# Kernel tuning notes

Measured on AMD Instinct MI355X. Metric: run time of the kernel, lower is better.

## Reference

```python
import jax, jax.numpy as jnp
import numpy as np

B, N, C = 2, 4096, 192
H = 8
D = C // H  # 24


def setup_inputs() -> dict:
    key = jax.random.key(0)
    k1, k2, k3, k4 = jax.random.split(key, 4)
    x = jax.random.normal(k1, (B, N, C), dtype=jnp.float32)
    # qkv Linear (no bias by default): torch Linear weight is [out, in] -> [3C, C]
    W_qkv = jax.random.normal(k2, (3 * C, C), dtype=jnp.float32) * (1.0 / np.sqrt(C))
    W_proj = jax.random.normal(k3, (C, C), dtype=jnp.float32) * (1.0 / np.sqrt(C))
    b_proj = jax.random.normal(k4, (C,), dtype=jnp.float32) * 0.01
    scale = jnp.asarray(D ** -0.5, dtype=jnp.float32)  # learned scalar, init head_dim**-0.5
    return {"x": x, "W_qkv": W_qkv, "W_proj": W_proj, "b_proj": b_proj, "scale": scale}


def reference(x, W_qkv, W_proj, b_proj, scale):
    b, n, c = x.shape
    h, d = H, c // H
    qkv = jnp.einsum('bnc,oc->bno', x, W_qkv)              # [B,N,3C]
    qkv = qkv.reshape(b, n, 3, h, d).transpose(2, 0, 3, 1, 4)  # [3,B,H,N,D]
    q, k, v = qkv[0], qkv[1], qkv[2]
    # (q_i - k_j).sum(-1) == sum(q_i) - sum(k_j): avoids the [B,H,N,N,D] blowup
    qs = q.sum(-1)                                          # [B,H,N]
    ks = k.sum(-1)                                          # [B,H,N]
    dist = qs[..., :, None] - ks[..., None, :]              # [B,H,N,N]
    attn = jax.nn.softmax(-dist * scale, axis=-1)           # [B,H,N,N]
    out = jnp.einsum('bhij,bhjd->bhid', attn, v)            # [B,H,N,D]
    out = out.transpose(0, 2, 1, 3).reshape(b, n, c)        # [B,N,C]
    return jnp.einsum('bnc,oc->bno', out, W_proj) + b_proj
```

## Files before the change

kernel.cpp:

```cpp
#include <hip/hip_runtime.h>

#define B 2
#define N 4096
#define C 192
#define H 8
#define D 24
#define ROWS 32
#define NCHUNK (B * N / ROWS)
#define PJ 1544

#define PART_OFF 0
#define XW_OFF   395264

__global__ __launch_bounds__(256) void kA(const float* __restrict__ x,
                                          const float* __restrict__ Wqkv,
                                          const float* __restrict__ scale,
                                          float* __restrict__ part) {
    __shared__ __align__(16) float wk[H * 196];
    __shared__ __align__(16) float lx[ROWS * 196];
    __shared__ float le[ROWS * 9];
    const int tid = threadIdx.x;
    const int blk = blockIdx.x;

    for (int i = tid; i < H * C; i += 256) {
        const int h = i / C, c = i - h * C;
        const float* wr = Wqkv + (size_t)(C + h * D) * C + c;
        float s = 0.f;
        #pragma unroll
        for (int d = 0; d < D; ++d) s += wr[d * C];
        wk[h * 196 + c] = s;
    }
    const float4* xb = (const float4*)(x + (size_t)blk * ROWS * C);
    #pragma unroll
    for (int k = 0; k < 6; ++k) {
        const int f4 = tid + k * 256;
        const int r = f4 / 48, c4 = f4 - r * 48;
        *(float4*)&lx[r * 196 + c4 * 4] = xb[f4];
    }
    __syncthreads();

    {
        const int r = tid >> 3, h = tid & 7;
        const float4* xr = (const float4*)&lx[r * 196];
        const float4* wh = (const float4*)&wk[h * 196];
        float acc = 0.f;
        #pragma unroll 8
        for (int c4 = 0; c4 < 48; ++c4) {
            float4 a = xr[c4], w = wh[c4];
            acc += a.x * w.x + a.y * w.y + a.z * w.z + a.w * w.w;
        }
        le[r * 9 + h] = __expf(acc * scale[0]);
    }
    __syncthreads();

    const int h = tid >> 5, c0 = tid & 31;
    float acc[6] = {};
    float zacc = 0.f;
    for (int r = 0; r < ROWS; ++r) {
        const float e = le[r * 9 + h];
        if (c0 == 0) zacc += e;
        #pragma unroll
        for (int j = 0; j < 6; ++j) acc[j] += e * lx[r * 196 + c0 + 32 * j];
    }
    float* pb = part + (size_t)blk * PJ;
    #pragma unroll
    for (int j = 0; j < 6; ++j) pb[h * C + c0 + 32 * j] = acc[j];
    if (c0 == 0) pb[1536 + h] = zacc;
}

__global__ __launch_bounds__(256) void kB(const float* __restrict__ part,
                                          float* __restrict__ xw) {
    const int i = blockIdx.x * 256 + threadIdx.x;
    if (i >= B * PJ) return;
    const int b = i / PJ, j = i - b * PJ;
    const float* p = part + (size_t)(b * 128) * PJ + j;
    float s0 = 0.f, s1 = 0.f, s2 = 0.f, s3 = 0.f;
    for (int ch = 0; ch < 128; ch += 4) {
        s0 += p[(size_t)(ch + 0) * PJ];
        s1 += p[(size_t)(ch + 1) * PJ];
        s2 += p[(size_t)(ch + 2) * PJ];
        s3 += p[(size_t)(ch + 3) * PJ];
    }
    xw[i] = (s0 + s1) + (s2 + s3);
}

__global__ __launch_bounds__(256) void kC(const float* __restrict__ Wqkv,
                                          const float* __restrict__ Wproj,
                                          const float* __restrict__ bproj,
                                          const float* __restrict__ xw,
                                          float* __restrict__ out) {
    __shared__ __align__(16) float lxw[PJ];
    __shared__ __align__(16) float lobar[C];
    __shared__ __align__(16) float ly[C];
    const int tid = threadIdx.x;
    const int blk = blockIdx.x;
    const int b = blk >> 7;

    for (int i = tid; i < PJ; i += 256) lxw[i] = xw[b * PJ + i];
    __syncthreads();

    if (tid < C) {
        const int h = tid / D;
        const float4* wv = (const float4*)(Wqkv + (size_t)(2 * C + tid) * C);
        const float4* xh = (const float4*)&lxw[h * C];
        float s = 0.f;
        #pragma unroll 8
        for (int c4 = 0; c4 < 48; ++c4) {
            float4 a = wv[c4], w = xh[c4];
            s += a.x * w.x + a.y * w.y + a.z * w.z + a.w * w.w;
        }
        lobar[tid] = s / lxw[1536 + h];
    }
    __syncthreads();

    if (tid < C) {
        const float4* wp = (const float4*)(Wproj + (size_t)tid * C);
        const float4* ob = (const float4*)lobar;
        float s = bproj[tid];
        #pragma unroll 8
        for (int c4 = 0; c4 < 48; ++c4) {
            float4 a = wp[c4], w = ob[c4];
            s += a.x * w.x + a.y * w.y + a.z * w.z + a.w * w.w;
        }
        ly[tid] = s;
    }
    __syncthreads();

    float4* o4 = (float4*)out + (size_t)blk * 1536;
    const float4* ly4 = (const float4*)ly;
    #pragma unroll
    for (int k = 0; k < 6; ++k) {
        const int f4 = tid + k * 256;
        o4[f4] = ly4[f4 % 48];
    }
}

extern "C" void kernel_launch(void* const* d_in, const int* in_sizes, int n_in,
                              void* d_out, int out_size, void* d_ws, size_t ws_size,
                              hipStream_t stream) {
    const float* x     = (const float*)d_in[0];
    const float* Wqkv  = (const float*)d_in[1];
    const float* Wproj = (const float*)d_in[2];
    const float* bproj = (const float*)d_in[3];
    const float* scale = (const float*)d_in[4];
    float* out  = (float*)d_out;
    float* ws   = (float*)d_ws;
    float* part = ws + PART_OFF;
    float* xw   = ws + XW_OFF;

    kA<<<NCHUNK, 256, 0, stream>>>(x, Wqkv, scale, part);
    kB<<<13,     256, 0, stream>>>(part, xw);
    kC<<<NCHUNK, 256, 0, stream>>>(Wqkv, Wproj, bproj, xw, out);
}
```

Measured before the change: 86.66 us.

## Fuse three kernels into one cooperative kernel with grid syncs

Merges the partial-sum, reduction, and output kernels into a single cooperative launch separated by grid-wide barriers, removing two kernel launch gaps. The middle reduction is also redistributed across all 256 blocks, with 8 lanes per output combined by shuffles, instead of 13 blocks each doing a long serial sum. The cost is the grid.sync overhead and the requirement that all 256 blocks be co-resident, which the cooperative launch must satisfy.

Result: slower. 156.6 us (+80.8%).

```diff
diff --git a/kernel.cpp b/kernel.cpp
--- a/kernel.cpp
+++ b/kernel.cpp
@@ -1,4 +1,7 @@
 #include <hip/hip_runtime.h>
+#include <hip/hip_cooperative_groups.h>
+
+namespace cg = cooperative_groups;
 
 #define B 2
 #define N 4096
@@ -12,13 +15,22 @@
 #define PART_OFF 0
 #define XW_OFF   395264
 
-__global__ __launch_bounds__(256) void kA(const float* __restrict__ x,
-                                          const float* __restrict__ Wqkv,
-                                          const float* __restrict__ scale,
-                                          float* __restrict__ part) {
+__global__ __launch_bounds__(256, 1) void k_fused(const float* __restrict__ x,
+                                                  const float* __restrict__ Wqkv,
+                                                  const float* __restrict__ Wproj,
+                                                  const float* __restrict__ bproj,
+                                                  const float* __restrict__ scale,
+                                                  float* __restrict__ part,
+                                                  float* __restrict__ xw,
+                                                  float* __restrict__ out) {
+    cg::grid_group grid = cg::this_grid();
     __shared__ __align__(16) float wk[H * 196];
     __shared__ __align__(16) float lx[ROWS * 196];
     __shared__ float le[ROWS * 9];
+    __shared__ __align__(16) float lxw[PJ];
+    __shared__ __align__(16) float lobar[C];
+    __shared__ __align__(16) float ly[C];
+
     const int tid = threadIdx.x;
     const int blk = blockIdx.x;
 
@@ -53,49 +65,43 @@
     }
     __syncthreads();
 
-    const int h = tid >> 5, c0 = tid & 31;
-    float acc[6] = {};
-    float zacc = 0.f;
-    for (int r = 0; r < ROWS; ++r) {
-        const float e = le[r * 9 + h];
-        if (c0 == 0) zacc += e;
+    {
+        const int h = tid >> 5, c0 = tid & 31;
+        float acc[6] = {};
+        float zacc = 0.f;
+        for (int r = 0; r < ROWS; ++r) {
+            const float e = le[r * 9 + h];
+            if (c0 == 0) zacc += e;
+            #pragma unroll
+            for (int j = 0; j < 6; ++j) acc[j] += e * lx[r * 196 + c0 + 32 * j];
+        }
+        float* pb = part + (size_t)blk * PJ;
         #pragma unroll
-        for (int j = 0; j < 6; ++j) acc[j] += e * lx[r * 196 + c0 + 32 * j];
+        for (int j = 0; j < 6; ++j) pb[h * C + c0 + 32 * j] = acc[j];
+        if (c0 == 0) pb[1536 + h] = zacc;
     }
-    float* pb = part + (size_t)blk * PJ;
-    #pragma unroll
-    for (int j = 0; j < 6; ++j) pb[h * C + c0 + 32 * j] = acc[j];
-    if (c0 == 0) pb[1536 + h] = zacc;
-}
 
-__global__ __launch_bounds__(256) void kB(const float* __restrict__ part,
-                                          float* __restrict__ xw) {
-    const int i = blockIdx.x * 256 + threadIdx.x;
-    if (i >= B * PJ) return;
-    const int b = i / PJ, j = i - b * PJ;
-    const float* p = part + (size_t)(b * 128) * PJ + j;
-    float s0 = 0.f, s1 = 0.f, s2 = 0.f, s3 = 0.f;
-    for (int ch = 0; ch < 128; ch += 4) {
-        s0 += p[(size_t)(ch + 0) * PJ];
-        s1 += p[(size_t)(ch + 1) * PJ];
-        s2 += p[(size_t)(ch + 2) * PJ];
-        s3 += p[(size_t)(ch + 3) * PJ];
+    grid.sync();
+
+    {
+        const int gid = blk * 256 + tid;
+        const int g = gid >> 3, li = gid & 7;
+        if (g < B * PJ) {
+            const int b = g / PJ, j = g - b * PJ;
+            const float* p = part + (size_t)(b * 128 + li) * PJ + j;
+            float s = 0.f;
+            #pragma unroll
+            for (int k = 0; k < 16; ++k) s += p[(size_t)(8 * k) * PJ];
+            s += __shfl_xor(s, 1);
+            s += __shfl_xor(s, 2);
+            s += __shfl_xor(s, 4);
+            if (li == 0) xw[g] = s;
+        }
     }
-    xw[i] = (s0 + s1) + (s2 + s3);
-}
 
-__global__ __launch_bounds__(256) void kC(const float* __restrict__ Wqkv,
-                                          const float* __restrict__ Wproj,
-                                          const float* __restrict__ bproj,
-                                          const float* __restrict__ xw,
-                                          float* __restrict__ out) {
-    __shared__ __align__(16) float lxw[PJ];
-    __shared__ __align__(16) float lobar[C];
-    __shared__ __align__(16) float ly[C];
-    const int tid = threadIdx.x;
-    const int blk = blockIdx.x;
+    grid.sync();
+
     const int b = blk >> 7;
-
     for (int i = tid; i < PJ; i += 256) lxw[i] = xw[b * PJ + i];
     __syncthreads();
 
@@ -148,7 +154,8 @@
     float* part = ws + PART_OFF;
     float* xw   = ws + XW_OFF;
 
-    kA<<<NCHUNK, 256, 0, stream>>>(x, Wqkv, scale, part);
-    kB<<<13,     256, 0, stream>>>(part, xw);
-    kC<<<NCHUNK, 256, 0, stream>>>(Wqkv, Wproj, bproj, xw, out);
+    void* args[] = {(void*)&x, (void*)&Wqkv, (void*)&Wproj, (void*)&bproj,
+                    (void*)&scale, (void*)&part, (void*)&xw, (void*)&out};
+    hipLaunchCooperativeKernel((const void*)k_fused, dim3(NCHUNK), dim3(256),
+                               args, 0, stream);
 }
```
